# Performance work log

Hardware: AMD Instinct MI355X
Metric: run time of the kernel (lower is better)

## Reference

```python
import jax, jax.numpy as jnp
import numpy as np

EPS = 1e-5

def _ln(x, g, b):
    m = jnp.mean(x, axis=-1, keepdims=True)
    v = jnp.var(x, axis=-1, keepdims=True)
    return (x - m) / jnp.sqrt(v + EPS) * g + b

def _lin(x, w, b):
    # torch-style weight [out, in]
    return x @ w.T + b

def _mlp(x, w1, b1, w2, b2):
    # Mlp: Linear -> exact GELU -> Linear (dropout=0)
    return _lin(jax.nn.gelu(_lin(x, w1, b1), approximate=False), w2, b2)

def setup_inputs() -> dict:
    B, C, H, W = 2, 256, 64, 64
    key = jax.random.key(0)
    ks = jax.random.split(key, 32)
    s = 0.02  # param init scale keeps attention logits in a sane range
    d = {
        'center_fea': jax.random.normal(ks[0], (B, C, H, W), jnp.float32),
        'wh_fea':     jax.random.normal(ks[1], (B, C, H, W), jnp.float32),
        'cls_fea':    jax.random.normal(ks[2], (B, C, H, W), jnp.float32),
        'mix_w': jax.random.normal(ks[3], (C, 3 * C), jnp.float32) * s,
        'mix_b': jnp.zeros((C,), jnp.float32),
        'ln_g': jnp.ones((C,), jnp.float32),
        'ln_b': jnp.zeros((C,), jnp.float32),
        'q1_w': jax.random.normal(ks[4], (C, C), jnp.float32) * s,
        'q1_b': jnp.zeros((C,), jnp.float32),
        'q2_w': jax.random.normal(ks[5], (C, C), jnp.float32) * s,
        'q2_b': jnp.zeros((C,), jnp.float32),
        'q3_w': jax.random.normal(ks[6], (C, C), jnp.float32) * s,
        'q3_b': jnp.zeros((C,), jnp.float32),
        'k_w': jax.random.normal(ks[7], (C, C), jnp.float32) * s,
        'k_b': jnp.zeros((C,), jnp.float32),
        'v_w': jax.random.normal(ks[8], (C, C), jnp.float32) * s,
        'v_b': jnp.zeros((C,), jnp.float32),
        'cmlp_w1': jax.random.normal(ks[9], (C, C), jnp.float32) * s,
        'cmlp_b1': jnp.zeros((C,), jnp.float32),
        'cmlp_w2': jax.random.normal(ks[10], (C, C), jnp.float32) * s,
        'cmlp_b2': jnp.zeros((C,), jnp.float32),
        'wmlp_w1': jax.random.normal(ks[11], (C, C), jnp.float32) * s,
        'wmlp_b1': jnp.zeros((C,), jnp.float32),
        'wmlp_w2': jax.random.normal(ks[12], (C, C), jnp.float32) * s,
        'wmlp_b2': jnp.zeros((C,), jnp.float32),
        'clsmlp_w1': jax.random.normal(ks[13], (C, C), jnp.float32) * s,
        'clsmlp_b1': jnp.zeros((C,), jnp.float32),
        'clsmlp_w2': jax.random.normal(ks[14], (C, C), jnp.float32) * s,
        'clsmlp_b2': jnp.zeros((C,), jnp.float32),
    }
    return d

def reference(center_fea, wh_fea, cls_fea, mix_w, mix_b, ln_g, ln_b,
              q1_w, q1_b, q2_w, q2_b, q3_w, q3_b, k_w, k_b, v_w, v_b,
              cmlp_w1, cmlp_b1, cmlp_w2, cmlp_b2,
              wmlp_w1, wmlp_b1, wmlp_w2, wmlp_b2,
              clsmlp_w1, clsmlp_b1, clsmlp_w2, clsmlp_b2):
    b, c, h, w = center_fea.shape
    # 1x1 conv mix over concatenated channels [b, 3c, h, w] -> [b, c, h, w]
    cat = jnp.concatenate([center_fea, wh_fea, cls_fea], axis=1)
    mix = jnp.einsum('oc,bchw->bohw', mix_w, cat) + mix_b[None, :, None, None]

    tok = lambda x: x.reshape(b, c, h * w).transpose(0, 2, 1)  # [b, N, c]
    cf, wf, clf, mf = tok(center_fea), tok(wh_fea), tok(cls_fea), tok(mix)

    ct, wt, clt, mt = _ln(cf, ln_g, ln_b), _ln(wf, ln_g, ln_b), _ln(clf, ln_g, ln_b), _ln(mf, ln_g, ln_b)

    kf = _lin(mt, k_w, k_b)  # shared K
    vf = _lin(mt, v_w, v_b)  # shared V

    def attend(q):
        score = jax.nn.softmax(jnp.einsum('bnd,bmd->bnm', q, kf), axis=-1)  # [b, N, N]
        return jnp.einsum('bnm,bmd->bnd', score, vf)

    cf  = _ln(cf  + attend(_lin(ct,  q1_w, q1_b)), ln_g, ln_b)
    wf  = _ln(wf  + attend(_lin(wt,  q2_w, q2_b)), ln_g, ln_b)
    clf = _ln(clf + attend(_lin(clt, q3_w, q3_b)), ln_g, ln_b)

    cf  = _ln(cf  + _mlp(cf,  cmlp_w1, cmlp_b1, cmlp_w2, cmlp_b2), ln_g, ln_b)
    wf  = _ln(wf  + _mlp(wf,  wmlp_w1, wmlp_b1, wmlp_w2, wmlp_b2), ln_g, ln_b)
    clf = _ln(clf + _mlp(clf, clsmlp_w1, clsmlp_b1, clsmlp_w2, clsmlp_b2), ln_g, ln_b)

    untok = lambda x: x.transpose(0, 2, 1).reshape(b, c, h, w)
    return (untok(cf), untok(wf), untok(clf))
```

## Files before the change

### kernel.cpp

```cpp
#include <hip/hip_runtime.h>
#include <hip/hip_bf16.h>
#include <math.h>

typedef unsigned int   u32;
typedef unsigned short u16;
typedef float floatx4 __attribute__((ext_vector_type(4)));
typedef short bf16x8  __attribute__((ext_vector_type(8)));

#define MFMA16(a,b,c) __builtin_amdgcn_mfma_f32_16x16x32_bf16((a),(b),(c),0,0,0)

static __device__ __forceinline__ float bfbits2f(u16 h){
    return __uint_as_float(((u32)h) << 16);
}
static __device__ __forceinline__ u16 f2bfbits(float f){
    u32 u = __float_as_uint(f);
    u32 r = (u + 0x7fffu + ((u >> 16) & 1u)) >> 16;
    return (u16)r;
}
static __device__ __forceinline__ bool sniff_bf16(const void* ln_g){
    return ((const u32*)ln_g)[0] == 0x3f803f80u;
}

struct PackJob { const void* src; void* dst; int n; int mode; };
struct PackParams { PackJob jobs[26]; const void* lng; };

__global__ __launch_bounds__(256) void k_pack(PackParams p){
    bool isb = sniff_bf16(p.lng);
    PackJob j = p.jobs[blockIdx.y];
    int i = blockIdx.x * 256 + threadIdx.x;
    if (i >= j.n) return;
    float v = isb ? bfbits2f(((const u16*)j.src)[i]) : ((const float*)j.src)[i];
    if (j.mode == 0) ((u16*)j.dst)[i]  = f2bfbits(v);
    else             ((float*)j.dst)[i] = v;
}

struct FtParams { const void* src[3]; u16* dst[3]; const void* lng; };

__global__ __launch_bounds__(256) void k_feat_t(FtParams p){
    bool isb = sniff_bf16(p.lng);
    int z = blockIdx.z; int si = z >> 1; int b = z & 1;
    const void* src = p.src[si]; u16* dst = p.dst[si];
    int n0 = blockIdx.x * 64, c0 = blockIdx.y * 64;
    __shared__ float tile[64][65];
    int t = threadIdx.x; int tx = t & 63; int ty = t >> 6;
    #pragma unroll
    for (int pp = 0; pp < 16; ++pp){
        int cl = ty + pp * 4;
        size_t off = ((size_t)b * 256 + c0 + cl) * 4096 + n0 + tx;
        float v = isb ? bfbits2f(((const u16*)src)[off]) : ((const float*)src)[off];
        tile[cl][tx] = v;
    }
    __syncthreads();
    #pragma unroll
    for (int pp = 0; pp < 16; ++pp){
        int nl = ty + pp * 4; int cl = tx;
        dst[((size_t)b * 4096 + n0 + nl) * 256 + c0 + cl] = f2bfbits(tile[cl][nl]);
    }
}

struct GemmJob { const u16* A0; const u16* A1; const u16* A2;
                 const u16* W; const float* bias; const u16* res; u16* out; };
struct GemmParams { GemmJob jobs[5]; int K; int op; };

__global__ __launch_bounds__(256, 4) void k_gemm(GemmParams p){
    GemmJob j = p.jobs[blockIdx.z];
    int m0 = blockIdx.x * 64, n0 = blockIdx.y * 64;
    __shared__ __align__(16) u16 As[64][72];
    __shared__ __align__(16) u16 Bs[64][72];
    int t = threadIdx.x;
    int wave = t >> 6, lane = t & 63, l15 = lane & 15, quad = lane >> 4;
    int mh = (wave & 1) * 32, nh = (wave >> 1) * 32;
    floatx4 acc[2][2];
    #pragma unroll
    for (int a = 0; a < 2; ++a)
        #pragma unroll
        for (int bq = 0; bq < 2; ++bq) acc[a][bq] = (floatx4){0.f,0.f,0.f,0.f};

    for (int k0 = 0; k0 < p.K; k0 += 64){
        __syncthreads();
        const u16* Ap = (k0 < 256) ? j.A0 : (k0 < 512 ? j.A1 : j.A2);
        int koff = k0 & 255;
        #pragma unroll
        for (int i = 0; i < 2; ++i){
            int idx = i * 256 + t; int r = idx >> 3; int sg = idx & 7;
            *(uint4*)&As[r][sg * 8] = *(const uint4*)(Ap + ((size_t)(m0 + r)) * 256 + koff + sg * 8);
            *(uint4*)&Bs[r][sg * 8] = *(const uint4*)(j.W + ((size_t)(n0 + r)) * p.K + k0 + sg * 8);
        }
        __syncthreads();
        #pragma unroll
        for (int kc = 0; kc < 2; ++kc){
            bf16x8 a0 = *(const bf16x8*)&As[mh +      l15][kc * 32 + quad * 8];
            bf16x8 a1 = *(const bf16x8*)&As[mh + 16 + l15][kc * 32 + quad * 8];
            bf16x8 b0 = *(const bf16x8*)&Bs[nh +      l15][kc * 32 + quad * 8];
            bf16x8 b1 = *(const bf16x8*)&Bs[nh + 16 + l15][kc * 32 + quad * 8];
            acc[0][0] = MFMA16(a0, b0, acc[0][0]);
            acc[0][1] = MFMA16(a0, b1, acc[0][1]);
            acc[1][0] = MFMA16(a1, b0, acc[1][0]);
            acc[1][1] = MFMA16(a1, b1, acc[1][1]);
        }
    }
    #pragma unroll
    for (int mb = 0; mb < 2; ++mb)
        #pragma unroll
        for (int nb = 0; nb < 2; ++nb){
            int col = n0 + nh + nb * 16 + l15;
            float bias = j.bias[col];
            #pragma unroll
            for (int rg = 0; rg < 4; ++rg){
                int row = m0 + mh + mb * 16 + quad * 4 + rg;
                float v = acc[mb][nb][rg] + bias;
                if (p.op == 1)      v = 0.5f * v * (1.0f + erff(v * 0.70710678118f));
                else if (p.op == 2) v += bfbits2f(j.res[(size_t)row * 256 + col]);
                j.out[(size_t)row * 256 + col] = f2bfbits(v);
            }
        }
}

struct LnJob { const u16* src; u16* dst; };
struct LnParams { LnJob jobs[4]; const float* g; const float* b; };

__global__ __launch_bounds__(256, 4) void k_ln(LnParams p){
    LnJob j = p.jobs[blockIdx.y];
    int wave = threadIdx.x >> 6, lane = threadIdx.x & 63;
    size_t tok = (size_t)blockIdx.x * 4 + wave;
    const u16* row = j.src + tok * 256;
    ushort4 raw = *(const ushort4*)(row + lane * 4);
    float v0 = bfbits2f(raw.x), v1 = bfbits2f(raw.y), v2 = bfbits2f(raw.z), v3 = bfbits2f(raw.w);
    float s1 = v0 + v1 + v2 + v3;
    float s2 = v0*v0 + v1*v1 + v2*v2 + v3*v3;
    #pragma unroll
    for (int off = 1; off < 64; off <<= 1){
        s1 += __shfl_xor(s1, off);
        s2 += __shfl_xor(s2, off);
    }
    float mean = s1 * (1.f/256.f);
    float var  = s2 * (1.f/256.f) - mean * mean;
    float rstd = rsqrtf(var + 1e-5f);
    int c = lane * 4;
    ushort4 o;
    o.x = f2bfbits((v0 - mean) * rstd * p.g[c+0] + p.b[c+0]);
    o.y = f2bfbits((v1 - mean) * rstd * p.g[c+1] + p.b[c+1]);
    o.z = f2bfbits((v2 - mean) * rstd * p.g[c+2] + p.b[c+2]);
    o.w = f2bfbits((v3 - mean) * rstd * p.g[c+3] + p.b[c+3]);
    *(ushort4*)(j.dst + tok * 256 + c) = o;
}

__global__ __launch_bounds__(256, 4) void k_vt(const u16* __restrict__ Vf, u16* __restrict__ Vt){
    int b = blockIdx.z;
    int n0 = blockIdx.x * 64, c0 = blockIdx.y * 64;
    __shared__ u16 tile[64][66];
    int t = threadIdx.x; int tx = t & 63; int ty = t >> 6;
    #pragma unroll
    for (int pp = 0; pp < 16; ++pp){
        int nl = ty + pp * 4;
        tile[nl][tx] = Vf[((size_t)b * 4096 + n0 + nl) * 256 + c0 + tx];
    }
    __syncthreads();
    #pragma unroll
    for (int pp = 0; pp < 16; ++pp){
        int cl = ty + pp * 4; int nl = tx;
        Vt[((size_t)b * 256 + c0 + cl) * 4096 + n0 + nl] = tile[nl][cl];
    }
}

struct FlashParams {
    const u16* Q[3]; const u16* K; const u16* Vt;
    const u16* Res[3]; u16* Out[3];
    const float* g; const float* b;
};

__global__ __launch_bounds__(256, 2) void k_flash(FlashParams p){
    int s = blockIdx.y >> 1, b = blockIdx.y & 1;
    int m0 = blockIdx.x * 64;
    const u16* Q   = p.Q[s]   + (size_t)b * 4096 * 256;
    const u16* Kf  = p.K      + (size_t)b * 4096 * 256;
    const u16* Vtg = p.Vt     + (size_t)b * 256 * 4096;
    const u16* Res = p.Res[s] + (size_t)b * 4096 * 256;
    u16*       Out = p.Out[s] + (size_t)b * 4096 * 256;

    __shared__ __align__(16) u16 Kl[64][264];
    __shared__ __align__(16) u16 Vh[128][72];
    __shared__ __align__(16) u16 Pl[4][16][72];

    int t = threadIdx.x, wave = t >> 6, lane = t & 63, l15 = lane & 15, quad = lane >> 4;

    bf16x8 qf[8];
    {
        const u16* qrow = Q + (size_t)(m0 + wave * 16 + l15) * 256 + quad * 8;
        #pragma unroll
        for (int kc = 0; kc < 8; ++kc) qf[kc] = *(const bf16x8*)(qrow + kc * 32);
    }
    floatx4 o[16];
    #pragma unroll
    for (int i = 0; i < 16; ++i) o[i] = (floatx4){0.f,0.f,0.f,0.f};
    float mrow[4] = {-INFINITY,-INFINITY,-INFINITY,-INFINITY};
    float lrow[4] = {0.f,0.f,0.f,0.f};

    for (int kv0 = 0; kv0 < 4096; kv0 += 64){
        __syncthreads();
        #pragma unroll
        for (int i = 0; i < 8; ++i){
            int idx = i * 256 + t; int r = idx >> 5; int sg = idx & 31;
            *(uint4*)&Kl[r][sg * 8] = *(const uint4*)(Kf + (size_t)(kv0 + r) * 256 + sg * 8);
        }
        #pragma unroll
        for (int i = 0; i < 4; ++i){
            int idx = i * 256 + t; int dl = idx >> 3; int sg = idx & 7;
            *(uint4*)&Vh[dl][sg * 8] = *(const uint4*)(Vtg + (size_t)dl * 4096 + kv0 + sg * 8);
        }
        __syncthreads();

        floatx4 sa[4];
        #pragma unroll
        for (int sub = 0; sub < 4; ++sub){
            sa[sub] = (floatx4){0.f,0.f,0.f,0.f};
            #pragma unroll
            for (int kc = 0; kc < 8; ++kc){
                bf16x8 kb = *(const bf16x8*)&Kl[sub * 16 + l15][kc * 32 + quad * 8];
                sa[sub] = MFMA16(qf[kc], kb, sa[sub]);
            }
        }
        float mx[4], al[4];
        #pragma unroll
        for (int rg = 0; rg < 4; ++rg){
            float m1 = fmaxf(fmaxf(sa[0][rg], sa[1][rg]), fmaxf(sa[2][rg], sa[3][rg]));
            m1 = fmaxf(m1, __shfl_xor(m1, 1));
            m1 = fmaxf(m1, __shfl_xor(m1, 2));
            m1 = fmaxf(m1, __shfl_xor(m1, 4));
            m1 = fmaxf(m1, __shfl_xor(m1, 8));
            float mn = fmaxf(mrow[rg], m1);
            al[rg] = __expf(mrow[rg] - mn);
            mrow[rg] = mn; mx[rg] = mn;
        }
        float rs[4] = {0.f,0.f,0.f,0.f};
        #pragma unroll
        for (int sub = 0; sub < 4; ++sub)
            #pragma unroll
            for (int rg = 0; rg < 4; ++rg){
                float pv = __expf(sa[sub][rg] - mx[rg]);
                sa[sub][rg] = pv;
                rs[rg] += pv;
            }
        #pragma unroll
        for (int rg = 0; rg < 4; ++rg){
            float r1 = rs[rg];
            r1 += __shfl_xor(r1, 1); r1 += __shfl_xor(r1, 2);
            r1 += __shfl_xor(r1, 4); r1 += __shfl_xor(r1, 8);
            lrow[rg] = lrow[rg] * al[rg] + r1;
        }
        #pragma unroll
        for (int dc = 0; dc < 16; ++dc)
            #pragma unroll
            for (int rg = 0; rg < 4; ++rg) o[dc][rg] *= al[rg];

        #pragma unroll
        for (int sub = 0; sub < 4; ++sub)
            #pragma unroll
            for (int rg = 0; rg < 4; ++rg)
                Pl[wave][quad * 4 + rg][sub * 16 + l15] = f2bfbits(sa[sub][rg]);
        __syncthreads();

        bf16x8 pa[2];
        pa[0] = *(const bf16x8*)&Pl[wave][l15][quad * 8];
        pa[1] = *(const bf16x8*)&Pl[wave][l15][32 + quad * 8];
        #pragma unroll
        for (int dc = 0; dc < 8; ++dc)
            #pragma unroll
            for (int k2 = 0; k2 < 2; ++k2){
                bf16x8 vb = *(const bf16x8*)&Vh[dc * 16 + l15][k2 * 32 + quad * 8];
                o[dc] = MFMA16(pa[k2], vb, o[dc]);
            }
        __syncthreads();
        #pragma unroll
        for (int i = 0; i < 4; ++i){
            int idx = i * 256 + t; int dl = idx >> 3; int sg = idx & 7;
            *(uint4*)&Vh[dl][sg * 8] = *(const uint4*)(Vtg + (size_t)(128 + dl) * 4096 + kv0 + sg * 8);
        }
        __syncthreads();
        #pragma unroll
        for (int dc = 0; dc < 8; ++dc)
            #pragma unroll
            for (int k2 = 0; k2 < 2; ++k2){
                bf16x8 vb = *(const bf16x8*)&Vh[dc * 16 + l15][k2 * 32 + quad * 8];
                o[8 + dc] = MFMA16(pa[k2], vb, o[8 + dc]);
            }
    }

    float inv[4];
    #pragma unroll
    for (int rg = 0; rg < 4; ++rg) inv[rg] = 1.0f / lrow[rg];
    float s1[4] = {0.f,0.f,0.f,0.f}, s2[4] = {0.f,0.f,0.f,0.f};
    #pragma unroll
    for (int dc = 0; dc < 16; ++dc)
        #pragma unroll
        for (int rg = 0; rg < 4; ++rg){
            int row = m0 + wave * 16 + quad * 4 + rg;
            float v = o[dc][rg] * inv[rg] + bfbits2f(Res[(size_t)row * 256 + dc * 16 + l15]);
            o[dc][rg] = v;
            s1[rg] += v; s2[rg] += v * v;
        }
    #pragma unroll
    for (int rg = 0; rg < 4; ++rg){
        float a = s1[rg], q2 = s2[rg];
        a  += __shfl_xor(a, 1);  a += __shfl_xor(a, 2);  a += __shfl_xor(a, 4);  a += __shfl_xor(a, 8);
        q2 += __shfl_xor(q2, 1); q2 += __shfl_xor(q2, 2); q2 += __shfl_xor(q2, 4); q2 += __shfl_xor(q2, 8);
        float mean = a * (1.f/256.f);
        float var  = q2 * (1.f/256.f) - mean * mean;
        s1[rg] = mean; s2[rg] = rsqrtf(var + 1e-5f);
    }
    #pragma unroll
    for (int dc = 0; dc < 16; ++dc){
        int c = dc * 16 + l15;
        float gv = p.g[c], bv = p.b[c];
        #pragma unroll
        for (int rg = 0; rg < 4; ++rg){
            int row = m0 + wave * 16 + quad * 4 + rg;
            Out[(size_t)row * 256 + c] = f2bfbits((o[dc][rg] - s1[rg]) * s2[rg] * gv + bv);
        }
    }
}

struct OutTParams { const u16* F[3]; void* out; const void* lng; };

__global__ __launch_bounds__(256, 4) void k_out_t(OutTParams p){
    bool isb = sniff_bf16(p.lng);
    int z = blockIdx.z; int s = z >> 1; int b = z & 1;
    const u16* F = p.F[s];
    int n0 = blockIdx.x * 64, c0 = blockIdx.y * 64;
    __shared__ u16 tile[64][66];
    int t = threadIdx.x; int tx = t & 63; int ty = t >> 6;
    #pragma unroll
    for (int pp = 0; pp < 16; ++pp){
        int nl = ty + pp * 4;
        tile[nl][tx] = F[((size_t)b * 4096 + n0 + nl) * 256 + c0 + tx];
    }
    __syncthreads();
    size_t obase = ((size_t)s * 2 + b) * 256 * 4096;
    #pragma unroll
    for (int pp = 0; pp < 16; ++pp){
        int cl = ty + pp * 4; int nl = tx;
        u16 raw = tile[nl][cl];
        size_t off = obase + (size_t)(c0 + cl) * 4096 + n0 + nl;
        if (isb) ((u16*)p.out)[off]   = raw;
        else     ((float*)p.out)[off] = bfbits2f(raw);
    }
}

extern "C" void kernel_launch(void* const* d_in, const int* in_sizes, int n_in,
                              void* d_out, int out_size, void* d_ws, size_t ws_size,
                              hipStream_t stream) {
    (void)in_sizes; (void)n_in; (void)out_size; (void)ws_size;
    const size_t SLOT = (size_t)2 * 4096 * 256;
    u16* ws = (u16*)d_ws;
    auto slot = [&](int i){ return ws + (size_t)i * SLOT; };

    u16 *Tc = slot(0),  *Tw = slot(1),  *Tcl = slot(2),  *Tm = slot(3);
    u16 *Lc = slot(4),  *Lw = slot(5),  *Lcl = slot(6),  *Lm = slot(7);
    u16 *Q1 = slot(8),  *Q2 = slot(9),  *Q3  = slot(10);
    u16 *Kf = slot(11), *Vf = slot(12), *Vt  = slot(13);
    u16 *Yc = slot(14), *Yw = slot(15), *Ycl = slot(16);
    u16 *Hc = Q1, *Hw = Q2, *Hcl = Q3;
    u16 *Zc = Lc, *Zw = Lw, *Zcl = Lcl;
    u16 *Fc = Kf, *Fw = Vf, *Fcl = Vt;

    u16* wbase = slot(17);
    u16 *mixw = wbase;
    u16 *q1w = wbase + 196608, *q2w = q1w + 65536, *q3w = q2w + 65536;
    u16 *kw  = q3w + 65536,    *vw  = kw  + 65536;
    u16 *cw1 = vw  + 65536, *cw2 = cw1 + 65536, *ww1 = cw2 + 65536,
        *ww2 = ww1 + 65536, *clw1 = ww2 + 65536, *clw2 = clw1 + 65536;
    float* pbase = (float*)(wbase + 1048576);
    float *mixb = pbase,        *lng = pbase+256,  *lnb = pbase+512,
          *q1b = pbase+768,  *q2b = pbase+1024, *q3b = pbase+1280,
          *kb  = pbase+1536, *vb  = pbase+1792,
          *cb1 = pbase+2048, *cb2 = pbase+2304, *wb1 = pbase+2560,
          *wb2 = pbase+2816, *clb1= pbase+3072, *clb2= pbase+3328;

    {
        PackParams pp;
        const int widx[12] = {3,7,9,11,13,15,17,19,21,23,25,27};
        u16* wdst[12] = {mixw,q1w,q2w,q3w,kw,vw,cw1,cw2,ww1,ww2,clw1,clw2};
        for (int i = 0; i < 12; ++i)
            pp.jobs[i] = PackJob{ d_in[widx[i]], wdst[i], (i==0?196608:65536), 0 };
        const int pidx[14] = {4,5,6,8,10,12,14,16,18,20,22,24,26,28};
        float* pdst[14] = {mixb,lng,lnb,q1b,q2b,q3b,kb,vb,cb1,cb2,wb1,wb2,clb1,clb2};
        for (int i = 0; i < 14; ++i)
            pp.jobs[12+i] = PackJob{ d_in[pidx[i]], pdst[i], 256, 1 };
        pp.lng = d_in[5];
        hipLaunchKernelGGL(k_pack, dim3(768, 26), dim3(256), 0, stream, pp);
    }
    {
        FtParams fp;
        fp.src[0] = d_in[0]; fp.src[1] = d_in[1]; fp.src[2] = d_in[2];
        fp.dst[0] = Tc; fp.dst[1] = Tw; fp.dst[2] = Tcl;
        fp.lng = d_in[5];
        hipLaunchKernelGGL(k_feat_t, dim3(64, 4, 6), dim3(256), 0, stream, fp);
    }
    {
        GemmParams gp; gp.K = 768; gp.op = 0;
        gp.jobs[0] = GemmJob{ Tc, Tw, Tcl, mixw, mixb, nullptr, Tm };
        hipLaunchKernelGGL(k_gemm, dim3(128, 4, 1), dim3(256), 0, stream, gp);
    }
    {
        LnParams lp; lp.g = lng; lp.b = lnb;
        lp.jobs[0] = LnJob{Tc, Lc}; lp.jobs[1] = LnJob{Tw, Lw};
        lp.jobs[2] = LnJob{Tcl, Lcl}; lp.jobs[3] = LnJob{Tm, Lm};
        hipLaunchKernelGGL(k_ln, dim3(2048, 4), dim3(256), 0, stream, lp);
    }
    {
        GemmParams gp; gp.K = 256; gp.op = 0;
        gp.jobs[0] = GemmJob{ Lc,  nullptr, nullptr, q1w, q1b, nullptr, Q1 };
        gp.jobs[1] = GemmJob{ Lw,  nullptr, nullptr, q2w, q2b, nullptr, Q2 };
        gp.jobs[2] = GemmJob{ Lcl, nullptr, nullptr, q3w, q3b, nullptr, Q3 };
        gp.jobs[3] = GemmJob{ Lm,  nullptr, nullptr, kw,  kb,  nullptr, Kf };
        gp.jobs[4] = GemmJob{ Lm,  nullptr, nullptr, vw,  vb,  nullptr, Vf };
        hipLaunchKernelGGL(k_gemm, dim3(128, 4, 5), dim3(256), 0, stream, gp);
    }
    hipLaunchKernelGGL(k_vt, dim3(64, 4, 2), dim3(256), 0, stream, Vf, Vt);
    {
        FlashParams fp;
        fp.Q[0] = Q1; fp.Q[1] = Q2; fp.Q[2] = Q3;
        fp.K = Kf; fp.Vt = Vt;
        fp.Res[0] = Tc; fp.Res[1] = Tw; fp.Res[2] = Tcl;
        fp.Out[0] = Yc; fp.Out[1] = Yw; fp.Out[2] = Ycl;
        fp.g = lng; fp.b = lnb;
        hipLaunchKernelGGL(k_flash, dim3(64, 6), dim3(256), 0, stream, fp);
    }
    {
        GemmParams gp; gp.K = 256; gp.op = 1;
        gp.jobs[0] = GemmJob{ Yc,  nullptr, nullptr, cw1,  cb1,  nullptr, Hc };
        gp.jobs[1] = GemmJob{ Yw,  nullptr, nullptr, ww1,  wb1,  nullptr, Hw };
        gp.jobs[2] = GemmJob{ Ycl, nullptr, nullptr, clw1, clb1, nullptr, Hcl };
        hipLaunchKernelGGL(k_gemm, dim3(128, 4, 3), dim3(256), 0, stream, gp);
    }
    {
        GemmParams gp; gp.K = 256; gp.op = 2;
        gp.jobs[0] = GemmJob{ Hc,  nullptr, nullptr, cw2,  cb2,  Yc,  Zc };
        gp.jobs[1] = GemmJob{ Hw,  nullptr, nullptr, ww2,  wb2,  Yw,  Zw };
        gp.jobs[2] = GemmJob{ Hcl, nullptr, nullptr, clw2, clb2, Ycl, Zcl };
        hipLaunchKernelGGL(k_gemm, dim3(128, 4, 3), dim3(256), 0, stream, gp);
    }
    {
        LnParams lp; lp.g = lng; lp.b = lnb;
        lp.jobs[0] = LnJob{Zc, Fc}; lp.jobs[1] = LnJob{Zw, Fw};
        lp.jobs[2] = LnJob{Zcl, Fcl}; lp.jobs[3] = LnJob{Zc, Fc};
        hipLaunchKernelGGL(k_ln, dim3(2048, 3), dim3(256), 0, stream, lp);
    }
    {
        OutTParams op;
        op.F[0] = Fc; op.F[1] = Fw; op.F[2] = Fcl;
        op.out = d_out; op.lng = d_in[5];
        hipLaunchKernelGGL(k_out_t, dim3(64, 4, 6), dim3(256), 0, stream, op);
    }
}
```

Baseline: 487.1 us.

## Restructure flash attention to share K/V tiles across three query streams with async LDS double-buffering

The flash-attention kernel now uses one block per 32-row query tile, with each of its three waves handling one of the three query streams (center, wh, cls), so every K/V tile loaded into LDS is reused by all three streams. K and V tiles are double-buffered and fetched with global_load_lds direct-to-LDS copies using an XOR swizzle. The P staging area reuses the current K buffer. The output rescale is skipped when no row max grows, and blocks are mapped to XCDs by batch to improve L2 locality. In exchange, the kernel runs 256 blocks of 192 threads at occupancy 1 with high register pressure (two 16-row halves of O per wave). This may leave the GPU underfilled and expose latency.

New measurement: 557.9 us. 1.15x slower.

```diff
diff --git a/kernel.cpp b/kernel.cpp
--- a/kernel.cpp
+++ b/kernel.cpp
@@ -19,6 +19,12 @@
 }
 static __device__ __forceinline__ bool sniff_bf16(const void* ln_g){
     return ((const u32*)ln_g)[0] == 0x3f803f80u;
+}
+
+typedef __attribute__((address_space(1))) const unsigned int gas_u32;
+typedef __attribute__((address_space(3))) unsigned int las_u32;
+static __device__ __forceinline__ void gl_lds16(const void* g, void* l){
+    __builtin_amdgcn_global_load_lds((gas_u32*)g, (las_u32*)l, 16, 0, 0);
 }
 
 struct PackJob { const void* src; void* dst; int n; int mode; };
@@ -169,153 +175,191 @@
     const float* g; const float* b;
 };
 
-__global__ __launch_bounds__(256, 2) void k_flash(FlashParams p){
-    int s = blockIdx.y >> 1, b = blockIdx.y & 1;
-    int m0 = blockIdx.x * 64;
-    const u16* Q   = p.Q[s]   + (size_t)b * 4096 * 256;
-    const u16* Kf  = p.K      + (size_t)b * 4096 * 256;
-    const u16* Vtg = p.Vt     + (size_t)b * 256 * 4096;
-    const u16* Res = p.Res[s] + (size_t)b * 4096 * 256;
-    u16*       Out = p.Out[s] + (size_t)b * 4096 * 256;
-
-    __shared__ __align__(16) u16 Kl[64][264];
-    __shared__ __align__(16) u16 Vh[128][72];
-    __shared__ __align__(16) u16 Pl[4][16][72];
-
-    int t = threadIdx.x, wave = t >> 6, lane = t & 63, l15 = lane & 15, quad = lane >> 4;
-
-    bf16x8 qf[8];
-    {
-        const u16* qrow = Q + (size_t)(m0 + wave * 16 + l15) * 256 + quad * 8;
-        #pragma unroll
-        for (int kc = 0; kc < 8; ++kc) qf[kc] = *(const bf16x8*)(qrow + kc * 32);
-    }
-    floatx4 o[16];
-    #pragma unroll
-    for (int i = 0; i < 16; ++i) o[i] = (floatx4){0.f,0.f,0.f,0.f};
-    float mrow[4] = {-INFINITY,-INFINITY,-INFINITY,-INFINITY};
-    float lrow[4] = {0.f,0.f,0.f,0.f};
-
-    for (int kv0 = 0; kv0 < 4096; kv0 += 64){
+__global__ __launch_bounds__(192, 1) void k_flash(FlashParams p){
+    int f = blockIdx.x;
+    int xcd = f & 7;
+    int b = xcd >> 2;
+    int tile = (xcd & 3) * 32 + (f >> 3);
+    int m0 = tile * 32;
+
+    int t = threadIdx.x, w = t >> 6, lane = t & 63, l15 = lane & 15, quad = lane >> 4;
+
+    const u16* Qg  = p.Q[w]   + (size_t)b * 4096 * 256;
+    const u16* Kg  = p.K      + (size_t)b * 4096 * 256;
+    const u16* Vg  = p.Vt     + (size_t)b * 256 * 4096;
+    const u16* Res = p.Res[w] + (size_t)b * 4096 * 256;
+    u16*       Out = p.Out[w] + (size_t)b * 4096 * 256;
+
+    __shared__ __align__(16) u16 Kb[2][64][256];
+    __shared__ __align__(16) u16 Vb[2][256][64];
+
+    auto stage = [&](int buf, int kv0){
+        #pragma unroll
+        for (int m = 0; m < 22; ++m){
+            int q = w + m * 3;
+            if (q < 32){
+                int r0 = q * 2 + (lane >> 5);
+                int gg = (lane & 31) ^ (r0 & 7);
+                gl_lds16(Kg + (size_t)(kv0 + r0) * 256 + gg * 8, &Kb[buf][q * 2][0]);
+            } else if (q < 64){
+                int j = q - 32;
+                int dl = j * 8 + (lane >> 3);
+                int gg = (lane & 7) ^ (dl & 7);
+                gl_lds16(Vg + (size_t)dl * 4096 + kv0 + gg * 8, &Vb[buf][j * 8][0]);
+            }
+        }
+    };
+
+    stage(0, 0);
+
+    bf16x8 qf[2][8];
+    #pragma unroll
+    for (int h = 0; h < 2; ++h){
+        const u16* qrow = Qg + (size_t)(m0 + h * 16 + l15) * 256 + quad * 8;
+        #pragma unroll
+        for (int kc = 0; kc < 8; ++kc) qf[h][kc] = *(const bf16x8*)(qrow + kc * 32);
+    }
+
+    floatx4 o[2][16];
+    #pragma unroll
+    for (int h = 0; h < 2; ++h)
+        #pragma unroll
+        for (int dc = 0; dc < 16; ++dc) o[h][dc] = (floatx4){0.f,0.f,0.f,0.f};
+    float mrow[2][4], lrow[2][4];
+    #pragma unroll
+    for (int h = 0; h < 2; ++h)
+        #pragma unroll
+        for (int rg = 0; rg < 4; ++rg){ mrow[h][rg] = -INFINITY; lrow[h][rg] = 0.f; }
+
+    __syncthreads();
+    int buf = 0;
+    int key = l15 & 7;
+
+    for (int tch = 0; tch < 64; ++tch){
+        if (tch < 63) stage(buf ^ 1, (tch + 1) * 64);
+        u16* Pb = &Kb[buf][0][0] + (size_t)w * (32 * 72);
+
+        floatx4 sa[2][4];
+        #pragma unroll
+        for (int h = 0; h < 2; ++h)
+            #pragma unroll
+            for (int sub = 0; sub < 4; ++sub) sa[h][sub] = (floatx4){0.f,0.f,0.f,0.f};
+        #pragma unroll
+        for (int sub = 0; sub < 4; ++sub){
+            int row = sub * 16 + l15;
+            #pragma unroll
+            for (int kc = 0; kc < 8; ++kc){
+                bf16x8 kb = *(const bf16x8*)&Kb[buf][row][((kc * 4 + quad) ^ key) * 8];
+                sa[0][sub] = MFMA16(qf[0][kc], kb, sa[0][sub]);
+                sa[1][sub] = MFMA16(qf[1][kc], kb, sa[1][sub]);
+            }
+        }
+
+        #pragma unroll
+        for (int h = 0; h < 2; ++h){
+            float al[4]; int grow = 0;
+            #pragma unroll
+            for (int rg = 0; rg < 4; ++rg){
+                float m1 = fmaxf(fmaxf(sa[h][0][rg], sa[h][1][rg]), fmaxf(sa[h][2][rg], sa[h][3][rg]));
+                m1 = fmaxf(m1, __shfl_xor(m1, 1));
+                m1 = fmaxf(m1, __shfl_xor(m1, 2));
+                m1 = fmaxf(m1, __shfl_xor(m1, 4));
+                m1 = fmaxf(m1, __shfl_xor(m1, 8));
+                grow |= (m1 > mrow[h][rg]) ? 1 : 0;
+                float mn = fmaxf(mrow[h][rg], m1);
+                al[rg] = __expf(mrow[h][rg] - mn);
+                mrow[h][rg] = mn;
+            }
+            float rs[4] = {0.f,0.f,0.f,0.f};
+            #pragma unroll
+            for (int sub = 0; sub < 4; ++sub)
+                #pragma unroll
+                for (int rg = 0; rg < 4; ++rg){
+                    float pv = __expf(sa[h][sub][rg] - mrow[h][rg]);
+                    sa[h][sub][rg] = pv;
+                    rs[rg] += pv;
+                }
+            #pragma unroll
+            for (int rg = 0; rg < 4; ++rg){
+                float r1 = rs[rg];
+                r1 += __shfl_xor(r1, 1); r1 += __shfl_xor(r1, 2);
+                r1 += __shfl_xor(r1, 4); r1 += __shfl_xor(r1, 8);
+                lrow[h][rg] = lrow[h][rg] * al[rg] + r1;
+            }
+            if (__any(grow)){
+                #pragma unroll
+                for (int dc = 0; dc < 16; ++dc)
+                    #pragma unroll
+                    for (int rg = 0; rg < 4; ++rg) o[h][dc][rg] *= al[rg];
+            }
+        }
+
+        asm volatile("s_waitcnt lgkmcnt(0)" ::: "memory");
+        __builtin_amdgcn_sched_barrier(0);
+        __builtin_amdgcn_s_barrier();
+
+        #pragma unroll
+        for (int h = 0; h < 2; ++h)
+            #pragma unroll
+            for (int sub = 0; sub < 4; ++sub)
+                #pragma unroll
+                for (int rg = 0; rg < 4; ++rg)
+                    Pb[(h * 16 + quad * 4 + rg) * 72 + sub * 16 + l15] = f2bfbits(sa[h][sub][rg]);
+
+        bf16x8 pa[2][2];
+        #pragma unroll
+        for (int h = 0; h < 2; ++h){
+            pa[h][0] = *(const bf16x8*)&Pb[(h * 16 + l15) * 72 + quad * 8];
+            pa[h][1] = *(const bf16x8*)&Pb[(h * 16 + l15) * 72 + 32 + quad * 8];
+        }
+        #pragma unroll
+        for (int dc = 0; dc < 16; ++dc){
+            int row = dc * 16 + l15;
+            #pragma unroll
+            for (int k2 = 0; k2 < 2; ++k2){
+                bf16x8 vb = *(const bf16x8*)&Vb[buf][row][((k2 * 4 + quad) ^ key) * 8];
+                o[0][dc] = MFMA16(pa[0][k2], vb, o[0][dc]);
+                o[1][dc] = MFMA16(pa[1][k2], vb, o[1][dc]);
+            }
+        }
+
         __syncthreads();
-        #pragma unroll
-        for (int i = 0; i < 8; ++i){
-            int idx = i * 256 + t; int r = idx >> 5; int sg = idx & 31;
-            *(uint4*)&Kl[r][sg * 8] = *(const uint4*)(Kf + (size_t)(kv0 + r) * 256 + sg * 8);
-        }
-        #pragma unroll
-        for (int i = 0; i < 4; ++i){
-            int idx = i * 256 + t; int dl = idx >> 3; int sg = idx & 7;
-            *(uint4*)&Vh[dl][sg * 8] = *(const uint4*)(Vtg + (size_t)dl * 4096 + kv0 + sg * 8);
-        }
-        __syncthreads();
-
-        floatx4 sa[4];
-        #pragma unroll
-        for (int sub = 0; sub < 4; ++sub){
-            sa[sub] = (floatx4){0.f,0.f,0.f,0.f};
-            #pragma unroll
-            for (int kc = 0; kc < 8; ++kc){
-                bf16x8 kb = *(const bf16x8*)&Kl[sub * 16 + l15][kc * 32 + quad * 8];
-                sa[sub] = MFMA16(qf[kc], kb, sa[sub]);
-            }
-        }
-        float mx[4], al[4];
+        buf ^= 1;
+    }
+
+    #pragma unroll
+    for (int h = 0; h < 2; ++h){
+        float inv[4];
+        #pragma unroll
+        for (int rg = 0; rg < 4; ++rg) inv[rg] = 1.0f / lrow[h][rg];
+        float s1[4] = {0.f,0.f,0.f,0.f}, s2[4] = {0.f,0.f,0.f,0.f};
+        #pragma unroll
+        for (int dc = 0; dc < 16; ++dc)
+            #pragma unroll
+            for (int rg = 0; rg < 4; ++rg){
+                int row = m0 + h * 16 + quad * 4 + rg;
+                float v = o[h][dc][rg] * inv[rg] + bfbits2f(Res[(size_t)row * 256 + dc * 16 + l15]);
+                o[h][dc][rg] = v;
+                s1[rg] += v; s2[rg] += v * v;
+            }
         #pragma unroll
         for (int rg = 0; rg < 4; ++rg){
-            float m1 = fmaxf(fmaxf(sa[0][rg], sa[1][rg]), fmaxf(sa[2][rg], sa[3][rg]));
-            m1 = fmaxf(m1, __shfl_xor(m1, 1));
-            m1 = fmaxf(m1, __shfl_xor(m1, 2));
-            m1 = fmaxf(m1, __shfl_xor(m1, 4));
-            m1 = fmaxf(m1, __shfl_xor(m1, 8));
-            float mn = fmaxf(mrow[rg], m1);
-            al[rg] = __expf(mrow[rg] - mn);
-            mrow[rg] = mn; mx[rg] = mn;
-        }
-        float rs[4] = {0.f,0.f,0.f,0.f};
-        #pragma unroll
-        for (int sub = 0; sub < 4; ++sub)
+            float a = s1[rg], q2 = s2[rg];
+            a  += __shfl_xor(a, 1);  a += __shfl_xor(a, 2);  a += __shfl_xor(a, 4);  a += __shfl_xor(a, 8);
+            q2 += __shfl_xor(q2, 1); q2 += __shfl_xor(q2, 2); q2 += __shfl_xor(q2, 4); q2 += __shfl_xor(q2, 8);
+            float mean = a * (1.f/256.f);
+            float var  = q2 * (1.f/256.f) - mean * mean;
+            s1[rg] = mean; s2[rg] = rsqrtf(var + 1e-5f);
+        }
+        #pragma unroll
+        for (int dc = 0; dc < 16; ++dc){
+            int c = dc * 16 + l15;
+            float gv = p.g[c], bv = p.b[c];
             #pragma unroll
             for (int rg = 0; rg < 4; ++rg){
-                float pv = __expf(sa[sub][rg] - mx[rg]);
-                sa[sub][rg] = pv;
-                rs[rg] += pv;
-            }
-        #pragma unroll
-        for (int rg = 0; rg < 4; ++rg){
-            float r1 = rs[rg];
-            r1 += __shfl_xor(r1, 1); r1 += __shfl_xor(r1, 2);
-            r1 += __shfl_xor(r1, 4); r1 += __shfl_xor(r1, 8);
-            lrow[rg] = lrow[rg] * al[rg] + r1;
-        }
-        #pragma unroll
-        for (int dc = 0; dc < 16; ++dc)
-            #pragma unroll
-            for (int rg = 0; rg < 4; ++rg) o[dc][rg] *= al[rg];
-
-        #pragma unroll
-        for (int sub = 0; sub < 4; ++sub)
-            #pragma unroll
-            for (int rg = 0; rg < 4; ++rg)
-                Pl[wave][quad * 4 + rg][sub * 16 + l15] = f2bfbits(sa[sub][rg]);
-        __syncthreads();
-
-        bf16x8 pa[2];
-        pa[0] = *(const bf16x8*)&Pl[wave][l15][quad * 8];
-        pa[1] = *(const bf16x8*)&Pl[wave][l15][32 + quad * 8];
-        #pragma unroll
-        for (int dc = 0; dc < 8; ++dc)
-            #pragma unroll
-            for (int k2 = 0; k2 < 2; ++k2){
-                bf16x8 vb = *(const bf16x8*)&Vh[dc * 16 + l15][k2 * 32 + quad * 8];
-                o[dc] = MFMA16(pa[k2], vb, o[dc]);
-            }
-        __syncthreads();
-        #pragma unroll
-        for (int i = 0; i < 4; ++i){
-            int idx = i * 256 + t; int dl = idx >> 3; int sg = idx & 7;
-            *(uint4*)&Vh[dl][sg * 8] = *(const uint4*)(Vtg + (size_t)(128 + dl) * 4096 + kv0 + sg * 8);
-        }
-        __syncthreads();
-        #pragma unroll
-        for (int dc = 0; dc < 8; ++dc)
-            #pragma unroll
-            for (int k2 = 0; k2 < 2; ++k2){
-                bf16x8 vb = *(const bf16x8*)&Vh[dc * 16 + l15][k2 * 32 + quad * 8];
-                o[8 + dc] = MFMA16(pa[k2], vb, o[8 + dc]);
-            }
-    }
-
-    float inv[4];
-    #pragma unroll
-    for (int rg = 0; rg < 4; ++rg) inv[rg] = 1.0f / lrow[rg];
-    float s1[4] = {0.f,0.f,0.f,0.f}, s2[4] = {0.f,0.f,0.f,0.f};
-    #pragma unroll
-    for (int dc = 0; dc < 16; ++dc)
-        #pragma unroll
-        for (int rg = 0; rg < 4; ++rg){
-            int row = m0 + wave * 16 + quad * 4 + rg;
-            float v = o[dc][rg] * inv[rg] + bfbits2f(Res[(size_t)row * 256 + dc * 16 + l15]);
-            o[dc][rg] = v;
-            s1[rg] += v; s2[rg] += v * v;
-        }
-    #pragma unroll
-    for (int rg = 0; rg < 4; ++rg){
-        float a = s1[rg], q2 = s2[rg];
-        a  += __shfl_xor(a, 1);  a += __shfl_xor(a, 2);  a += __shfl_xor(a, 4);  a += __shfl_xor(a, 8);
-        q2 += __shfl_xor(q2, 1); q2 += __shfl_xor(q2, 2); q2 += __shfl_xor(q2, 4); q2 += __shfl_xor(q2, 8);
-        float mean = a * (1.f/256.f);
-        float var  = q2 * (1.f/256.f) - mean * mean;
-        s1[rg] = mean; s2[rg] = rsqrtf(var + 1e-5f);
-    }
-    #pragma unroll
-    for (int dc = 0; dc < 16; ++dc){
-        int c = dc * 16 + l15;
-        float gv = p.g[c], bv = p.b[c];
-        #pragma unroll
-        for (int rg = 0; rg < 4; ++rg){
-            int row = m0 + wave * 16 + quad * 4 + rg;
-            Out[(size_t)row * 256 + c] = f2bfbits((o[dc][rg] - s1[rg]) * s2[rg] * gv + bv);
+                int row = m0 + h * 16 + quad * 4 + rg;
+                Out[(size_t)row * 256 + c] = f2bfbits((o[h][dc][rg] - s1[rg]) * s2[rg] * gv + bv);
+            }
         }
     }
 }
@@ -424,7 +468,7 @@
         fp.Res[0] = Tc; fp.Res[1] = Tw; fp.Res[2] = Tcl;
         fp.Out[0] = Yc; fp.Out[1] = Yw; fp.Out[2] = Ycl;
         fp.g = lng; fp.b = lnb;
-        hipLaunchKernelGGL(k_flash, dim3(64, 6), dim3(256), 0, stream, fp);
+        hipLaunchKernelGGL(k_flash, dim3(256), dim3(192), 0, stream, fp);
     }
     {
         GemmParams gp; gp.K = 256; gp.op = 1;
```

## Prefetch K/V tiles into registers and stage full V tile in LDS

Applied to the files above, without the earlier changes.

Global loads for the next K and V tiles are issued into registers before the current tile's compute, so load latency overlaps the MFMA work. V is staged as a whole 256-row tile in LDS instead of two 128-row halves, which removes two block barriers per iteration. The block-wide barrier around the per-wave P tile is replaced by an LDS waitcnt and a scheduling barrier. Rescaling of the output accumulator is skipped when no row max grew. In exchange the kernel uses 64 more registers per thread for the prefetch buffers and more LDS, which may lower occupancy under launch_bounds(256,2).

Result: slower. 853.0 us (+75.1%).

```diff
diff --git a/kernel.cpp b/kernel.cpp
--- a/kernel.cpp
+++ b/kernel.cpp
@@ -179,7 +179,7 @@
     u16*       Out = p.Out[s] + (size_t)b * 4096 * 256;
 
     __shared__ __align__(16) u16 Kl[64][264];
-    __shared__ __align__(16) u16 Vh[128][72];
+    __shared__ __align__(16) u16 Vh[256][72];
     __shared__ __align__(16) u16 Pl[4][16][72];
 
     int t = threadIdx.x, wave = t >> 6, lane = t & 63, l15 = lane & 15, quad = lane >> 4;
@@ -196,19 +196,35 @@
     float mrow[4] = {-INFINITY,-INFINITY,-INFINITY,-INFINITY};
     float lrow[4] = {0.f,0.f,0.f,0.f};
 
-    for (int kv0 = 0; kv0 < 4096; kv0 += 64){
-        __syncthreads();
+    uint4 kreg[8], vreg[8];
+    auto issue = [&](int kv0){
         #pragma unroll
         for (int i = 0; i < 8; ++i){
             int idx = i * 256 + t; int r = idx >> 5; int sg = idx & 31;
-            *(uint4*)&Kl[r][sg * 8] = *(const uint4*)(Kf + (size_t)(kv0 + r) * 256 + sg * 8);
-        }
-        #pragma unroll
-        for (int i = 0; i < 4; ++i){
+            kreg[i] = *(const uint4*)(Kf + (size_t)(kv0 + r) * 256 + sg * 8);
+        }
+        #pragma unroll
+        for (int i = 0; i < 8; ++i){
             int idx = i * 256 + t; int dl = idx >> 3; int sg = idx & 7;
-            *(uint4*)&Vh[dl][sg * 8] = *(const uint4*)(Vtg + (size_t)dl * 4096 + kv0 + sg * 8);
-        }
+            vreg[i] = *(const uint4*)(Vtg + (size_t)dl * 4096 + kv0 + sg * 8);
+        }
+    };
+    issue(0);
+
+    for (int kvc = 0; kvc < 64; ++kvc){
         __syncthreads();
+        #pragma unroll
+        for (int i = 0; i < 8; ++i){
+            int idx = i * 256 + t; int r = idx >> 5; int sg = idx & 31;
+            *(uint4*)&Kl[r][sg * 8] = kreg[i];
+        }
+        #pragma unroll
+        for (int i = 0; i < 8; ++i){
+            int idx = i * 256 + t; int dl = idx >> 3; int sg = idx & 7;
+            *(uint4*)&Vh[dl][sg * 8] = vreg[i];
+        }
+        __syncthreads();
+        if (kvc < 63) issue((kvc + 1) * 64);
 
         floatx4 sa[4];
         #pragma unroll
@@ -220,7 +236,7 @@
                 sa[sub] = MFMA16(qf[kc], kb, sa[sub]);
             }
         }
-        float mx[4], al[4];
+        float al[4]; int grow = 0;
         #pragma unroll
         for (int rg = 0; rg < 4; ++rg){
             float m1 = fmaxf(fmaxf(sa[0][rg], sa[1][rg]), fmaxf(sa[2][rg], sa[3][rg]));
@@ -228,16 +244,17 @@
             m1 = fmaxf(m1, __shfl_xor(m1, 2));
             m1 = fmaxf(m1, __shfl_xor(m1, 4));
             m1 = fmaxf(m1, __shfl_xor(m1, 8));
+            grow |= (m1 > mrow[rg]) ? 1 : 0;
             float mn = fmaxf(mrow[rg], m1);
             al[rg] = __expf(mrow[rg] - mn);
-            mrow[rg] = mn; mx[rg] = mn;
+            mrow[rg] = mn;
         }
         float rs[4] = {0.f,0.f,0.f,0.f};
         #pragma unroll
         for (int sub = 0; sub < 4; ++sub)
             #pragma unroll
             for (int rg = 0; rg < 4; ++rg){
-                float pv = __expf(sa[sub][rg] - mx[rg]);
+                float pv = __expf(sa[sub][rg] - mrow[rg]);
                 sa[sub][rg] = pv;
                 rs[rg] += pv;
             }
@@ -248,42 +265,30 @@
             r1 += __shfl_xor(r1, 4); r1 += __shfl_xor(r1, 8);
             lrow[rg] = lrow[rg] * al[rg] + r1;
         }
-        #pragma unroll
-        for (int dc = 0; dc < 16; ++dc)
+        if (__any(grow)){
             #pragma unroll
-            for (int rg = 0; rg < 4; ++rg) o[dc][rg] *= al[rg];
+            for (int dc = 0; dc < 16; ++dc)
+                #pragma unroll
+                for (int rg = 0; rg < 4; ++rg) o[dc][rg] *= al[rg];
+        }
 
         #pragma unroll
         for (int sub = 0; sub < 4; ++sub)
             #pragma unroll
             for (int rg = 0; rg < 4; ++rg)
                 Pl[wave][quad * 4 + rg][sub * 16 + l15] = f2bfbits(sa[sub][rg]);
-        __syncthreads();
-
-        bf16x8 pa[2];
-        pa[0] = *(const bf16x8*)&Pl[wave][l15][quad * 8];
-        pa[1] = *(const bf16x8*)&Pl[wave][l15][32 + quad * 8];
-        #pragma unroll
-        for (int dc = 0; dc < 8; ++dc)
-            #pragma unroll
-            for (int k2 = 0; k2 < 2; ++k2){
-                bf16x8 vb = *(const bf16x8*)&Vh[dc * 16 + l15][k2 * 32 + quad * 8];
-                o[dc] = MFMA16(pa[k2], vb, o[dc]);
-            }
-        __syncthreads();
-        #pragma unroll
-        for (int i = 0; i < 4; ++i){
-            int idx = i * 256 + t; int dl = idx >> 3; int sg = idx & 7;
-            *(uint4*)&Vh[dl][sg * 8] = *(const uint4*)(Vtg + (size_t)(128 + dl) * 4096 + kv0 + sg * 8);
-        }
-        __syncthreads();
-        #pragma unroll
-        for (int dc = 0; dc < 8; ++dc)
-            #pragma unroll
-            for (int k2 = 0; k2 < 2; ++k2){
-                bf16x8 vb = *(const bf16x8*)&Vh[dc * 16 + l15][k2 * 32 + quad * 8];
-                o[8 + dc] = MFMA16(pa[k2], vb, o[8 + dc]);
-            }
+        asm volatile("s_waitcnt lgkmcnt(0)" ::: "memory");
+        __builtin_amdgcn_sched_barrier(0);
+
+        bf16x8 pa0 = *(const bf16x8*)&Pl[wave][l15][quad * 8];
+        bf16x8 pa1 = *(const bf16x8*)&Pl[wave][l15][32 + quad * 8];
+        #pragma unroll
+        for (int dc = 0; dc < 16; ++dc){
+            bf16x8 vb0 = *(const bf16x8*)&Vh[dc * 16 + l15][quad * 8];
+            bf16x8 vb1 = *(const bf16x8*)&Vh[dc * 16 + l15][32 + quad * 8];
+            o[dc] = MFMA16(pa0, vb0, o[dc]);
+            o[dc] = MFMA16(pa1, vb1, o[dc]);
+        }
     }
 
     float inv[4];
```
